# Optimization experiments

Hardware: AMD Instinct MI355X
Metric: run time of the kernel (lower is better)

## Reference

```python
import jax, jax.numpy as jnp
import numpy as np

N = 30000          # mesh vertices
B = 5 * 16         # p_bins * t_bins geodesic patch bins
NEURONS = [16, 64, 64, 32]


def setup_inputs() -> dict:
    key = jax.random.key(0)
    ks = jax.random.split(key, 7)
    x = jax.random.normal(ks[0], (N, NEURONS[0]), dtype=jnp.float32)
    conn = jax.random.randint(ks[1], (N, B), 0, N)  # per-vertex per-bin source index
    s1 = 1.0 / np.sqrt(NEURONS[0])
    W1 = jax.random.uniform(ks[2], (NEURONS[0], NEURONS[1]), minval=-s1, maxval=s1, dtype=jnp.float32)
    s2 = 1.0 / np.sqrt(B * NEURONS[1])
    Wg1 = jax.random.uniform(ks[3], (B, NEURONS[1], NEURONS[2]), minval=-s2, maxval=s2, dtype=jnp.float32)
    b1 = jax.random.uniform(ks[4], (NEURONS[2],), minval=-s2, maxval=s2, dtype=jnp.float32)
    s3 = 1.0 / np.sqrt(B * NEURONS[2])
    Wg2 = jax.random.uniform(ks[5], (B, NEURONS[2], NEURONS[3]), minval=-s3, maxval=s3, dtype=jnp.float32)
    b2 = jax.random.uniform(ks[6], (NEURONS[3],), minval=-s3, maxval=s3, dtype=jnp.float32)
    return {"x": x, "W1": W1, "Wg1": Wg1, "b1": b1, "Wg2": Wg2, "b2": b2, "conn": conn}


def _geodesic(h, conn, Wg, b):
    # gather geodesic patch: [N, B, C_in], then per-bin contraction
    patches = h[conn]                               # irregular gather
    return jnp.einsum("nbi,bio->no", patches, Wg) + b


def reference(x, W1, Wg1, b1, Wg2, b2, conn):
    h = jax.nn.relu(x @ W1)                         # linear_1 (no bias, l_bias=False)
    h = jax.nn.relu(_geodesic(h, conn, Wg1, b1))    # GC_1 + relu
    res = _geodesic(h, conn, Wg2, b2)               # GC_2
    norm = jnp.linalg.norm(res, axis=-1, keepdims=True)
    return res / norm
```

## Files before the change

kernel.cpp:

```cpp
#include <hip/hip_runtime.h>
#include <stdint.h>
#include <stddef.h>


typedef __attribute__((ext_vector_type(8))) short bf16x8;
typedef __attribute__((ext_vector_type(4))) float f32x4;

#define BINS 80
#define SPLITK 4
#define BPC 20
#define PF 6

static __device__ __forceinline__ unsigned short f2bf(float f) {
  union { float f; unsigned int u; } c; c.f = f;
  unsigned int u = c.u;
  return (unsigned short)((u + 0x7FFFu + ((u >> 16) & 1u)) >> 16);
}

static __device__ __forceinline__ void wait_vm(int m) {
  if (m >= 12)      asm volatile("s_waitcnt vmcnt(12)");
  else if (m == 10) asm volatile("s_waitcnt vmcnt(10)");
  else if (m == 8)  asm volatile("s_waitcnt vmcnt(8)");
  else if (m == 6)  asm volatile("s_waitcnt vmcnt(6)");
  else if (m == 4)  asm volatile("s_waitcnt vmcnt(4)");
  else if (m == 2)  asm volatile("s_waitcnt vmcnt(2)");
  else              asm volatile("s_waitcnt vmcnt(0)");
}

__global__ __launch_bounds__(256) void k_lin1(const float* __restrict__ x,
                                              const float* __restrict__ W1,
                                              unsigned short* __restrict__ h1b, int n) {
  __shared__ float w1s[16 * 64];
  int tid = threadIdx.x;
  for (int i = tid; i < 16 * 64; i += 256) w1s[i] = W1[i];
  __syncthreads();
  int v = blockIdx.x * 256 + tid;
  if (v >= n) return;
  const float4* xp = (const float4*)(x + (size_t)v * 16);
  float4 x0 = xp[0], x1 = xp[1], x2 = xp[2], x3 = xp[3];
  float xr[16] = {x0.x, x0.y, x0.z, x0.w, x1.x, x1.y, x1.z, x1.w,
                  x2.x, x2.y, x2.z, x2.w, x3.x, x3.y, x3.z, x3.w};
  float acc[64];
#pragma unroll
  for (int o = 0; o < 64; ++o) acc[o] = 0.f;
#pragma unroll
  for (int i = 0; i < 16; ++i) {
    float xi = xr[i];
#pragma unroll
    for (int o = 0; o < 64; ++o) acc[o] = fmaf(xi, w1s[i * 64 + o], acc[o]);
  }
  unsigned short* hr = h1b + (size_t)v * 64;
#pragma unroll
  for (int o8 = 0; o8 < 8; ++o8) {
    bf16x8 pack;
#pragma unroll
    for (int j = 0; j < 8; ++j) pack[j] = (short)f2bf(fmaxf(acc[o8 * 8 + j], 0.f));
    *(bf16x8*)(hr + o8 * 8) = pack;
  }
}

__global__ __launch_bounds__(256) void k_wimg(const float* __restrict__ Wg,
                                              unsigned char* __restrict__ img,
                                              int O, int total) {
  int t = blockIdx.x * 256 + threadIdx.x;
  if (t >= total) return;
  int j = t & 3;
  int r = t >> 2;
  int o = r % O;
  int r2 = r / O;
  int z = r2 & 1;
  int b = r2 >> 1;
  bf16x8 pack;
#pragma unroll
  for (int tt = 0; tt < 8; ++tt)
    pack[tt] = (short)f2bf(Wg[(size_t)(b * 64 + z * 32 + j * 8 + tt) * O + o]);
  size_t boff = (size_t)b * (O * 128) + z * (O * 64) + o * 64 + ((j + (o >> 1)) & 3) * 16;
  *(bf16x8*)(img + boff) = pack;
}

template <int OT>
__global__ __launch_bounds__(512, 1) void k_geo3(const unsigned short* __restrict__ hin,
                                                 const unsigned char* __restrict__ wimg,
                                                 const int* __restrict__ conn,
                                                 float* __restrict__ part, int n) {
  constexpr int SLAB = OT * 1024;
  constexpr int R = (BPC * SLAB) / 8192;
  __shared__ alignas(16) unsigned char wg_s[BPC * SLAB];
  __shared__ int conn_s[256 * 21];

  const int tid = threadIdx.x;
  const int lane = tid & 63;
  const int wave = tid >> 6;
  const int ln15 = lane & 15;
  const int lq = lane >> 4;
  const int v0 = blockIdx.x * 256;
  const int chunk = blockIdx.y;
  const int bin0 = chunk * BPC;

  for (int t = tid; t < 256 * BPC; t += 512) {
    int v = t / BPC, c = t - v * BPC;
    int vv = v0 + v;
    if (vv > n - 1) vv = n - 1;
    conn_s[v * 21 + c] = conn[(size_t)vv * BINS + bin0 + c];
  }

  auto stage = [&](int ph) {
#pragma unroll
    for (int r = 0; r < R; ++r) {
      int off = (r * 512 + tid) * 16;
      int bin = off / SLAB;
      int within = off & (SLAB - 1);
      __builtin_amdgcn_global_load_lds(
          (const __attribute__((address_space(1))) unsigned int*)(const void*)
              (wimg + (size_t)(bin0 + bin) * (2 * SLAB) + ph * SLAB + within),
          (__attribute__((address_space(3))) unsigned int*)(void*)(wg_s + off),
          16, 0, 0);
    }
  };

  int boffs[OT];
#pragma unroll
  for (int ot = 0; ot < OT; ++ot) {
    int o = ot * 16 + ln15;
    boffs[ot] = o * 64 + ((lq + (o >> 1)) & 3) * 16;
  }

  const int crow0 = (wave * 32 + ln15) * 21;
  const int crow1 = crow0 + 16 * 21;
  const int koff = lq * 8;

  bf16x8 As[8][2];
  f32x4 acc[2][OT];
#pragma unroll
  for (int mt = 0; mt < 2; ++mt)
#pragma unroll
    for (int ot = 0; ot < OT; ++ot) acc[mt][ot] = (f32x4){0.f, 0.f, 0.f, 0.f};

#define ISSUE(ph, j) do {                                                        \
    int c0_ = conn_s[crow0 + (j)];                                               \
    int c1_ = conn_s[crow1 + (j)];                                               \
    const void* p0_ = (const void*)(hin + (size_t)c0_ * 64 + (ph) * 32 + koff);  \
    const void* p1_ = (const void*)(hin + (size_t)c1_ * 64 + (ph) * 32 + koff);  \
    asm volatile("global_load_dwordx4 %0, %1, off" : "=v"(As[(j) & 7][0]) : "v"(p0_)); \
    asm volatile("global_load_dwordx4 %0, %1, off" : "=v"(As[(j) & 7][1]) : "v"(p1_)); \
  } while (0)

  auto run_phase = [&](int ph) {
#pragma unroll
    for (int b = 0; b < BPC; ++b) {
      if (b + PF < BPC) ISSUE(ph, b + PF);
      int rem = BPC - 1 - b;
      wait_vm(2 * (rem > PF ? PF : rem));
      __builtin_amdgcn_sched_barrier(0);
      const unsigned char* wb = wg_s + b * SLAB;
#pragma unroll
      for (int ot = 0; ot < OT; ++ot) {
        bf16x8 bf = *(const bf16x8*)(wb + boffs[ot]);
        acc[0][ot] = __builtin_amdgcn_mfma_f32_16x16x32_bf16(As[b & 7][0], bf, acc[0][ot], 0, 0, 0);
        acc[1][ot] = __builtin_amdgcn_mfma_f32_16x16x32_bf16(As[b & 7][1], bf, acc[1][ot], 0, 0, 0);
      }
    }
  };

  stage(0);
  __syncthreads();
#pragma unroll
  for (int j = 0; j < PF; ++j) ISSUE(0, j);
  run_phase(0);

  asm volatile("s_waitcnt lgkmcnt(0)" ::: "memory");
  __builtin_amdgcn_s_barrier();
  __builtin_amdgcn_sched_barrier(0);
  stage(1);
#pragma unroll
  for (int j = 0; j < PF; ++j) ISSUE(1, j);
  asm volatile("s_waitcnt vmcnt(0)" ::: "memory");
  __builtin_amdgcn_s_barrier();
  __builtin_amdgcn_sched_barrier(0);
  run_phase(1);
#undef ISSUE

  constexpr int O = OT * 16;
  float* pbase = part + (size_t)chunk * n * O;
#pragma unroll
  for (int mt = 0; mt < 2; ++mt)
#pragma unroll
    for (int ot = 0; ot < OT; ++ot)
#pragma unroll
      for (int r = 0; r < 4; ++r) {
        int v = v0 + wave * 32 + mt * 16 + lq * 4 + r;
        if (v < n) pbase[(size_t)v * O + ot * 16 + ln15] = acc[mt][ot][r];
      }
}

__global__ __launch_bounds__(256) void k_fin1(const float* __restrict__ part,
                                              const float* __restrict__ bias,
                                              unsigned short* __restrict__ out, int n) {
  int t = blockIdx.x * 256 + threadIdx.x;
  int total = n * 16;
  if (t >= total) return;
  int base = t * 4;
  int o = base & 63;
  size_t stride = (size_t)n * 64;
  const float* p = part + base;
  float4 s = *(const float4*)(p);
#pragma unroll
  for (int c = 1; c < SPLITK; ++c) {
    float4 q = *(const float4*)(p + c * stride);
    s.x += q.x; s.y += q.y; s.z += q.z; s.w += q.w;
  }
  float4 b4 = *(const float4*)(bias + o);
  ushort4 pack;
  pack.x = f2bf(fmaxf(s.x + b4.x, 0.f));
  pack.y = f2bf(fmaxf(s.y + b4.y, 0.f));
  pack.z = f2bf(fmaxf(s.z + b4.z, 0.f));
  pack.w = f2bf(fmaxf(s.w + b4.w, 0.f));
  *(ushort4*)(out + base) = pack;
}

__global__ __launch_bounds__(256) void k_fin2(const float* __restrict__ part,
                                              const float* __restrict__ bias,
                                              float* __restrict__ out, int n) {
  int v = blockIdx.x * 16 + (threadIdx.x >> 4);
  int o = threadIdx.x & 15;
  if (v >= n) return;
  size_t stride = (size_t)n * 32;
  const float* p = part + (size_t)v * 32 + o;
  float a = 0.f, b = 0.f;
#pragma unroll
  for (int c = 0; c < SPLITK; ++c) {
    a += p[c * stride];
    b += p[c * stride + 16];
  }
  a += bias[o];
  b += bias[o + 16];
  float ss = a * a + b * b;
  ss += __shfl_xor(ss, 1);
  ss += __shfl_xor(ss, 2);
  ss += __shfl_xor(ss, 4);
  ss += __shfl_xor(ss, 8);
  float inv = 1.0f / sqrtf(ss);
  out[(size_t)v * 32 + o] = a * inv;
  out[(size_t)v * 32 + 16 + o] = b * inv;
}

extern "C" void kernel_launch(void* const* d_in, const int* in_sizes, int n_in,
                              void* d_out, int out_size, void* d_ws, size_t ws_size,
                              hipStream_t stream) {
  const float* x   = (const float*)d_in[0];
  const float* W1  = (const float*)d_in[1];
  const float* Wg1 = (const float*)d_in[2];
  const float* b1  = (const float*)d_in[3];
  const float* Wg2 = (const float*)d_in[4];
  const float* b2  = (const float*)d_in[5];
  const int*  conn = (const int*)d_in[6];
  int n = in_sizes[0] / 16;

  unsigned char* ws = (unsigned char*)d_ws;
  size_t hb = ((size_t)n * 64 * 2 + 255) & ~(size_t)255;
  unsigned short* h1b = (unsigned short*)(ws);
  unsigned short* h2b = (unsigned short*)(ws + hb);
  unsigned char*  w1i = ws + 2 * hb;
  unsigned char*  w2i = ws + 2 * hb + 80 * 8192;
  float* part = (float*)(ws + 2 * hb + 80 * 8192 + 80 * 4096);

  k_wimg<<<(80 * 2 * 64 * 4 + 255) / 256, 256, 0, stream>>>(Wg1, w1i, 64, 80 * 2 * 64 * 4);
  k_wimg<<<(80 * 2 * 32 * 4 + 255) / 256, 256, 0, stream>>>(Wg2, w2i, 32, 80 * 2 * 32 * 4);
  k_lin1<<<(n + 255) / 256, 256, 0, stream>>>(x, W1, h1b, n);

  int vt = (n + 255) / 256;
  k_geo3<4><<<dim3(vt, SPLITK), 512, 0, stream>>>(h1b, w1i, conn, part, n);
  k_fin1<<<(n * 16 + 255) / 256, 256, 0, stream>>>(part, b1, h2b, n);
  k_geo3<2><<<dim3(vt, SPLITK), 512, 0, stream>>>(h2b, w2i, conn, part, n);
  k_fin2<<<(n + 15) / 16, 256, 0, stream>>>(part, b2, (float*)d_out, n);
}
```

Before: 131.7 us.

## Keep conn indices in registers, raise occupancy, split layer-2 bins eight ways

Removes the shared-memory connectivity table and instead loads each thread's neighbour indices directly into packed 16-bit registers. Launch bounds now allow several blocks per CU, and the second geodesic layer splits its bins across eight chunks for more parallelism. Partial-sum traffic uses non-temporal loads and stores, and the weight staging overlaps the first gather prefetch. The 16-bit packing assumes vertex indices below 65536, and the extra split increases partial-sum reduction traffic.

```diff
diff --git a/kernel.cpp b/kernel.cpp
--- a/kernel.cpp
+++ b/kernel.cpp
@@ -7,9 +7,9 @@
 typedef __attribute__((ext_vector_type(4))) float f32x4;
 
 #define BINS 80
-#define SPLITK 4
-#define BPC 20
-#define PF 6
+#define SPLITK1 4
+#define SPLITK2 8
+#define PFD 5
 
 static __device__ __forceinline__ unsigned short f2bf(float f) {
   union { float f; unsigned int u; } c; c.f = f;
@@ -18,8 +18,7 @@
 }
 
 static __device__ __forceinline__ void wait_vm(int m) {
-  if (m >= 12)      asm volatile("s_waitcnt vmcnt(12)");
-  else if (m == 10) asm volatile("s_waitcnt vmcnt(10)");
+  if (m >= 10)      asm volatile("s_waitcnt vmcnt(10)");
   else if (m == 8)  asm volatile("s_waitcnt vmcnt(8)");
   else if (m == 6)  asm volatile("s_waitcnt vmcnt(6)");
   else if (m == 4)  asm volatile("s_waitcnt vmcnt(4)");
@@ -78,15 +77,15 @@
   *(bf16x8*)(img + boff) = pack;
 }
 
-template <int OT>
-__global__ __launch_bounds__(512, 1) void k_geo3(const unsigned short* __restrict__ hin,
+template <int OT, int BPCT>
+__global__ __launch_bounds__(512, 4) void k_geo4(const unsigned short* __restrict__ hin,
                                                  const unsigned char* __restrict__ wimg,
                                                  const int* __restrict__ conn,
                                                  float* __restrict__ part, int n) {
   constexpr int SLAB = OT * 1024;
-  constexpr int R = (BPC * SLAB) / 8192;
-  __shared__ alignas(16) unsigned char wg_s[BPC * SLAB];
-  __shared__ int conn_s[256 * 21];
+  constexpr int TOT = BPCT * SLAB;
+  constexpr int RR = (TOT + 8191) / 8192;
+  __shared__ alignas(16) unsigned char wg_s[TOT];
 
   const int tid = threadIdx.x;
   const int lane = tid & 63;
@@ -94,29 +93,37 @@
   const int ln15 = lane & 15;
   const int lq = lane >> 4;
   const int v0 = blockIdx.x * 256;
-  const int chunk = blockIdx.y;
-  const int bin0 = chunk * BPC;
-
-  for (int t = tid; t < 256 * BPC; t += 512) {
-    int v = t / BPC, c = t - v * BPC;
-    int vv = v0 + v;
-    if (vv > n - 1) vv = n - 1;
-    conn_s[v * 21 + c] = conn[(size_t)vv * BINS + bin0 + c];
-  }
+  const int bin0 = blockIdx.y * BPCT;
+
+  int vv0 = v0 + wave * 32 + ln15;      if (vv0 > n - 1) vv0 = n - 1;
+  int vv1 = v0 + wave * 32 + 16 + ln15; if (vv1 > n - 1) vv1 = n - 1;
 
   auto stage = [&](int ph) {
 #pragma unroll
-    for (int r = 0; r < R; ++r) {
+    for (int r = 0; r < RR; ++r) {
       int off = (r * 512 + tid) * 16;
-      int bin = off / SLAB;
-      int within = off & (SLAB - 1);
-      __builtin_amdgcn_global_load_lds(
-          (const __attribute__((address_space(1))) unsigned int*)(const void*)
-              (wimg + (size_t)(bin0 + bin) * (2 * SLAB) + ph * SLAB + within),
-          (__attribute__((address_space(3))) unsigned int*)(void*)(wg_s + off),
-          16, 0, 0);
+      if (off < TOT) {
+        int bin = off / SLAB;
+        int within = off & (SLAB - 1);
+        __builtin_amdgcn_global_load_lds(
+            (const __attribute__((address_space(1))) unsigned int*)(const void*)
+                (wimg + (size_t)(bin0 + bin) * (2 * SLAB) + ph * SLAB + within),
+            (__attribute__((address_space(3))) unsigned int*)(void*)(wg_s + off),
+            16, 0, 0);
+      }
     }
   };
+
+  stage(0);
+
+  unsigned int cpk[BPCT];
+#pragma unroll
+  for (int j = 0; j < BPCT; ++j) {
+    int c0 = __builtin_nontemporal_load(conn + (size_t)vv0 * BINS + bin0 + j);
+    int c1 = __builtin_nontemporal_load(conn + (size_t)vv1 * BINS + bin0 + j);
+    cpk[j] = ((unsigned)c0 & 0xffffu) | ((unsigned)c1 << 16);
+  }
+  __builtin_amdgcn_sched_barrier(0);
 
   int boffs[OT];
 #pragma unroll
@@ -125,11 +132,9 @@
     boffs[ot] = o * 64 + ((lq + (o >> 1)) & 3) * 16;
   }
 
-  const int crow0 = (wave * 32 + ln15) * 21;
-  const int crow1 = crow0 + 16 * 21;
   const int koff = lq * 8;
 
-  bf16x8 As[8][2];
+  bf16x8 As[6][2];
   f32x4 acc[2][OT];
 #pragma unroll
   for (int mt = 0; mt < 2; ++mt)
@@ -137,35 +142,36 @@
     for (int ot = 0; ot < OT; ++ot) acc[mt][ot] = (f32x4){0.f, 0.f, 0.f, 0.f};
 
 #define ISSUE(ph, j) do {                                                        \
-    int c0_ = conn_s[crow0 + (j)];                                               \
-    int c1_ = conn_s[crow1 + (j)];                                               \
+    int c0_ = (int)(cpk[(j)] & 0xffffu);                                         \
+    int c1_ = (int)(cpk[(j)] >> 16);                                             \
     const void* p0_ = (const void*)(hin + (size_t)c0_ * 64 + (ph) * 32 + koff);  \
     const void* p1_ = (const void*)(hin + (size_t)c1_ * 64 + (ph) * 32 + koff);  \
-    asm volatile("global_load_dwordx4 %0, %1, off" : "=v"(As[(j) & 7][0]) : "v"(p0_)); \
-    asm volatile("global_load_dwordx4 %0, %1, off" : "=v"(As[(j) & 7][1]) : "v"(p1_)); \
+    asm volatile("global_load_dwordx4 %0, %1, off" : "=v"(As[(j) % 6][0]) : "v"(p0_)); \
+    asm volatile("global_load_dwordx4 %0, %1, off" : "=v"(As[(j) % 6][1]) : "v"(p1_)); \
   } while (0)
 
   auto run_phase = [&](int ph) {
 #pragma unroll
-    for (int b = 0; b < BPC; ++b) {
-      if (b + PF < BPC) ISSUE(ph, b + PF);
-      int rem = BPC - 1 - b;
-      wait_vm(2 * (rem > PF ? PF : rem));
+    for (int b = 0; b < BPCT; ++b) {
+      if (b + PFD < BPCT) ISSUE(ph, b + PFD);
+      int rem = BPCT - 1 - b;
+      wait_vm(2 * (rem > PFD ? PFD : rem));
       __builtin_amdgcn_sched_barrier(0);
       const unsigned char* wb = wg_s + b * SLAB;
 #pragma unroll
       for (int ot = 0; ot < OT; ++ot) {
         bf16x8 bf = *(const bf16x8*)(wb + boffs[ot]);
-        acc[0][ot] = __builtin_amdgcn_mfma_f32_16x16x32_bf16(As[b & 7][0], bf, acc[0][ot], 0, 0, 0);
-        acc[1][ot] = __builtin_amdgcn_mfma_f32_16x16x32_bf16(As[b & 7][1], bf, acc[1][ot], 0, 0, 0);
+        acc[0][ot] = __builtin_amdgcn_mfma_f32_16x16x32_bf16(As[b % 6][0], bf, acc[0][ot], 0, 0, 0);
+        acc[1][ot] = __builtin_amdgcn_mfma_f32_16x16x32_bf16(As[b % 6][1], bf, acc[1][ot], 0, 0, 0);
       }
     }
   };
 
-  stage(0);
-  __syncthreads();
-#pragma unroll
-  for (int j = 0; j < PF; ++j) ISSUE(0, j);
+#pragma unroll
+  for (int j = 0; j < PFD; ++j) ISSUE(0, j);
+  wait_vm(2 * PFD);
+  __builtin_amdgcn_s_barrier();
+  __builtin_amdgcn_sched_barrier(0);
   run_phase(0);
 
   asm volatile("s_waitcnt lgkmcnt(0)" ::: "memory");
@@ -173,15 +179,15 @@
   __builtin_amdgcn_sched_barrier(0);
   stage(1);
 #pragma unroll
-  for (int j = 0; j < PF; ++j) ISSUE(1, j);
-  asm volatile("s_waitcnt vmcnt(0)" ::: "memory");
+  for (int j = 0; j < PFD; ++j) ISSUE(1, j);
+  wait_vm(2 * PFD);
   __builtin_amdgcn_s_barrier();
   __builtin_amdgcn_sched_barrier(0);
   run_phase(1);
 #undef ISSUE
 
   constexpr int O = OT * 16;
-  float* pbase = part + (size_t)chunk * n * O;
+  float* pbase = part + (size_t)blockIdx.y * n * O;
 #pragma unroll
   for (int mt = 0; mt < 2; ++mt)
 #pragma unroll
@@ -189,7 +195,9 @@
 #pragma unroll
       for (int r = 0; r < 4; ++r) {
         int v = v0 + wave * 32 + mt * 16 + lq * 4 + r;
-        if (v < n) pbase[(size_t)v * O + ot * 16 + ln15] = acc[mt][ot][r];
+        if (v < n)
+          __builtin_nontemporal_store(acc[mt][ot][r],
+                                      pbase + (size_t)v * O + ot * 16 + ln15);
       }
 }
 
@@ -203,18 +211,18 @@
   int o = base & 63;
   size_t stride = (size_t)n * 64;
   const float* p = part + base;
-  float4 s = *(const float4*)(p);
-#pragma unroll
-  for (int c = 1; c < SPLITK; ++c) {
-    float4 q = *(const float4*)(p + c * stride);
-    s.x += q.x; s.y += q.y; s.z += q.z; s.w += q.w;
-  }
-  float4 b4 = *(const float4*)(bias + o);
+  f32x4 s = __builtin_nontemporal_load((const f32x4*)(p));
+#pragma unroll
+  for (int c = 1; c < SPLITK1; ++c) {
+    f32x4 q = __builtin_nontemporal_load((const f32x4*)(p + c * stride));
+    s += q;
+  }
+  const float* b4 = bias + o;
   ushort4 pack;
-  pack.x = f2bf(fmaxf(s.x + b4.x, 0.f));
-  pack.y = f2bf(fmaxf(s.y + b4.y, 0.f));
-  pack.z = f2bf(fmaxf(s.z + b4.z, 0.f));
-  pack.w = f2bf(fmaxf(s.w + b4.w, 0.f));
+  pack.x = f2bf(fmaxf(s[0] + b4[0], 0.f));
+  pack.y = f2bf(fmaxf(s[1] + b4[1], 0.f));
+  pack.z = f2bf(fmaxf(s[2] + b4[2], 0.f));
+  pack.w = f2bf(fmaxf(s[3] + b4[3], 0.f));
   *(ushort4*)(out + base) = pack;
 }
 
@@ -228,9 +236,9 @@
   const float* p = part + (size_t)v * 32 + o;
   float a = 0.f, b = 0.f;
 #pragma unroll
-  for (int c = 0; c < SPLITK; ++c) {
-    a += p[c * stride];
-    b += p[c * stride + 16];
+  for (int c = 0; c < SPLITK2; ++c) {
+    a += __builtin_nontemporal_load(p + c * stride);
+    b += __builtin_nontemporal_load(p + c * stride + 16);
   }
   a += bias[o];
   b += bias[o + 16];
@@ -269,8 +277,8 @@
   k_lin1<<<(n + 255) / 256, 256, 0, stream>>>(x, W1, h1b, n);
 
   int vt = (n + 255) / 256;
-  k_geo3<4><<<dim3(vt, SPLITK), 512, 0, stream>>>(h1b, w1i, conn, part, n);
+  k_geo4<4, 20><<<dim3(vt, SPLITK1), 512, 0, stream>>>(h1b, w1i, conn, part, n);
   k_fin1<<<(n * 16 + 255) / 256, 256, 0, stream>>>(part, b1, h2b, n);
-  k_geo3<2><<<dim3(vt, SPLITK), 512, 0, stream>>>(h2b, w2i, conn, part, n);
+  k_geo4<2, 10><<<dim3(vt, SPLITK2), 512, 0, stream>>>(h2b, w2i, conn, part, n);
   k_fin2<<<(n + 15) / 16, 256, 0, stream>>>(part, b2, (float*)d_out, n);
 }
```

After: 171.4 us. 30.1% more time.
